# Optimization experiments

Measured on AMD Instinct MI355X. Metric: run time of the kernel, lower is better.

## Reference

```python
import jax, jax.numpy as jnp
import numpy as np

D = 2048
N_PASSES = 2
TOKENS = 16384


def _wht_matrix(d):
    # Sylvester construction of the (unnormalized) Walsh-Hadamard matrix.
    h = np.array([[1.0]], dtype=np.float32)
    while h.shape[0] < d:
        h = np.block([[h, h], [h, -h]])
    return jnp.asarray(h)


def setup_inputs() -> dict:
    key = jax.random.key(0)
    kx, ks = jax.random.split(key)
    x = jax.random.normal(kx, (TOKENS, D), dtype=jnp.float32)
    # random +/-1 sign arrays, one per pass (buffers in the torch module)
    signs = (2 * jax.random.randint(ks, (N_PASSES, D), 0, 2) - 1).astype(jnp.int32)
    wht_mat = _wht_matrix(D)
    return {"x": x, "signs": signs, "wht_mat": wht_mat}


def reference(x, signs, wht_mat):
    # Cascaded SRHT: (sign flip -> dense WHT matmul) x n_passes, scale fused at end.
    final_scale = jnp.asarray(1.0 / (D ** (N_PASSES / 2.0)), dtype=x.dtype)
    s = signs.astype(x.dtype)
    out = x
    for i in range(N_PASSES):
        out = out * s[i]          # [tokens, d] broadcast sign flip
        out = out @ wht_mat       # [tokens, d] x [d, d]
    return out * final_scale
```

## Files before the change

### kernel.cpp

```cpp
#include <hip/hip_runtime.h>

#define DIM 2048

__device__ __forceinline__ int sw(int e) {
  return e ^ (((e >> 7) & 7) << 2);
}

__device__ __forceinline__ float4 sign_flip(float4 v, uint4 s) {
  float4 r;
  r.x = __uint_as_float(__float_as_uint(v.x) ^ (s.x & 0x80000000u));
  r.y = __uint_as_float(__float_as_uint(v.y) ^ (s.y & 0x80000000u));
  r.z = __uint_as_float(__float_as_uint(v.z) ^ (s.z & 0x80000000u));
  r.w = __uint_as_float(__float_as_uint(v.w) ^ (s.w & 0x80000000u));
  return r;
}

#define BFLY(a, b) { float _t = (a); (a) = _t + (b); (b) = _t - (b); }

__device__ __forceinline__ void bf4_pair(float4 &a, float4 &b) {
  BFLY(a.x, b.x); BFLY(a.y, b.y); BFLY(a.z, b.z); BFLY(a.w, b.w);
}

__device__ __forceinline__ void bf_comps(float4 &a) {
  BFLY(a.x, a.y); BFLY(a.z, a.w);
  BFLY(a.x, a.z); BFLY(a.y, a.w);
}

__device__ __forceinline__ void bf_oct(float4 v[8]) {
  bf4_pair(v[0], v[1]); bf4_pair(v[2], v[3]);
  bf4_pair(v[4], v[5]); bf4_pair(v[6], v[7]);
  bf4_pair(v[0], v[2]); bf4_pair(v[1], v[3]);
  bf4_pair(v[4], v[6]); bf4_pair(v[5], v[7]);
  bf4_pair(v[0], v[4]); bf4_pair(v[1], v[5]);
  bf4_pair(v[2], v[6]); bf4_pair(v[3], v[7]);
}

template <int CTRL>
__device__ __forceinline__ float dpp_mov(float x) {
  return __int_as_float(
      __builtin_amdgcn_mov_dpp(__float_as_int(x), CTRL, 0xF, 0xF, true));
}

template <int CTRL>
__device__ __forceinline__ void dpp_stage(float4 v[8], float sgn) {
  #pragma unroll
  for (int i = 0; i < 8; ++i) {
    float px = dpp_mov<CTRL>(v[i].x);
    float py = dpp_mov<CTRL>(v[i].y);
    float pz = dpp_mov<CTRL>(v[i].z);
    float pw = dpp_mov<CTRL>(v[i].w);
    v[i].x = fmaf(sgn, v[i].x, px);
    v[i].y = fmaf(sgn, v[i].y, py);
    v[i].z = fmaf(sgn, v[i].z, pz);
    v[i].w = fmaf(sgn, v[i].w, pw);
  }
}

__global__ __launch_bounds__(256) void srht2_kernel(
    const float* __restrict__ x, const int* __restrict__ signs,
    float* __restrict__ out, int nrows) {
  __shared__ __align__(16) float lds[4][DIM];
  const int lane = threadIdx.x & 63;
  const int wv   = threadIdx.x >> 6;
  const int row  = blockIdx.x * 4 + wv;

  const float sgn1 = (lane & 1) ? -1.0f : 1.0f;
  const float sgn2 = (lane & 2) ? -1.0f : 1.0f;

  const float4* __restrict__ xr = (const float4*)(x + (size_t)row * DIM);
  const uint4*  __restrict__ s0 = (const uint4*)signs;

  float4 v[8];
  #pragma unroll
  for (int c = 0; c < 8; ++c) v[c] = xr[c * 64 + lane];
  #pragma unroll
  for (int c = 0; c < 8; ++c) v[c] = sign_flip(v[c], s0[c * 64 + lane]);

  #pragma unroll
  for (int c = 0; c < 8; ++c) bf_comps(v[c]);
  bf_oct(v);
  dpp_stage<0xB1>(v, sgn1);
  dpp_stage<0x4E>(v, sgn2);

  float* L = lds[wv];
  #pragma unroll
  for (int c = 0; c < 8; ++c)
    *(float4*)(L + sw(c * 256 + lane * 4)) = v[c];
  __syncthreads();

  const int rbase = (((lane >> 1) & 1) << 2) | (((lane >> 2) & 1) << 3)
                  | ((lane & 1) << 7) | ((lane >> 3) << 8);
  float4 w[8];
  #pragma unroll
  for (int j = 0; j < 8; ++j)
    w[j] = *(const float4*)(L + sw(rbase + (j << 4)));

  bf_oct(w);
  dpp_stage<0xB1>(w, sgn1);

  const uint4* __restrict__ s1 = (const uint4*)(signs + DIM);
  #pragma unroll
  for (int j = 0; j < 8; ++j)
    w[j] = sign_flip(w[j], s1[(rbase >> 2) + (j << 2)]);

  #pragma unroll
  for (int j = 0; j < 8; ++j) bf_comps(w[j]);
  bf_oct(w);
  dpp_stage<0xB1>(w, sgn1);
  dpp_stage<0x4E>(w, sgn2);

  __syncthreads();
  #pragma unroll
  for (int j = 0; j < 8; ++j)
    *(float4*)(L + sw(rbase + (j << 4))) = w[j];
  __syncthreads();

  const int rb2 = ((lane & 1) << 3) | (((lane >> 1) & 1) << 2)
                | (((lane >> 2) & 1) << 4) | (((lane >> 3) & 1) << 5)
                | (((lane >> 4) & 1) << 6) | (((lane >> 5) & 1) << 7);
  #pragma unroll
  for (int c = 0; c < 8; ++c)
    v[c] = *(const float4*)(L + sw(rb2 + (c << 8)));

  bf_oct(v);
  dpp_stage<0xB1>(v, sgn1);

  const float sc = 1.0f / 2048.0f;
  float4* __restrict__ orow = (float4*)(out + (size_t)row * DIM);
  #pragma unroll
  for (int c = 0; c < 8; ++c) {
    float4 t = v[c];
    t.x *= sc; t.y *= sc; t.z *= sc; t.w *= sc;
    orow[(rb2 >> 2) + (c << 6)] = t;
  }
}

extern "C" void kernel_launch(void* const* d_in, const int* in_sizes, int n_in,
                              void* d_out, int out_size, void* d_ws, size_t ws_size,
                              hipStream_t stream) {
  const float* x     = (const float*)d_in[0];
  const int*   signs = (const int*)d_in[1];
  float*       out   = (float*)d_out;
  const int nrows   = in_sizes[0] / DIM;
  const int nblocks = nrows / 4;
  hipLaunchKernelGGL(srht2_kernel, dim3(nblocks), dim3(256), 0, stream,
                     x, signs, out, nrows);
}
```

Before: 239.7 us.

## Make waves persistent with register prefetch of next row and packed sign masks

Each wave now runs as a persistent worker that processes several rows with a grid-stride loop, prefetching the next row into registers while it computes the current one. Sign vectors are loaded once per wave and packed into 32-bit bitmasks, so per-row sign loads go away. Block-wide __syncthreads is replaced by wave barriers, since each wave owns its own LDS slice, and output uses nontemporal stores. This costs more registers, which may lower occupancy, and rows_per_wave assumes nrows divides evenly by 4096 waves.

Result: slower. 245.4 us (+2.4%).

```diff
diff --git a/kernel.cpp b/kernel.cpp
--- a/kernel.cpp
+++ b/kernel.cpp
@@ -1,18 +1,20 @@
 #include <hip/hip_runtime.h>
 
 #define DIM 2048
+
+typedef float fvec4 __attribute__((ext_vector_type(4)));
 
 __device__ __forceinline__ int sw(int e) {
   return e ^ (((e >> 7) & 7) << 2);
 }
 
-__device__ __forceinline__ float4 sign_flip(float4 v, uint4 s) {
-  float4 r;
-  r.x = __uint_as_float(__float_as_uint(v.x) ^ (s.x & 0x80000000u));
-  r.y = __uint_as_float(__float_as_uint(v.y) ^ (s.y & 0x80000000u));
-  r.z = __uint_as_float(__float_as_uint(v.z) ^ (s.z & 0x80000000u));
-  r.w = __uint_as_float(__float_as_uint(v.w) ^ (s.w & 0x80000000u));
-  return r;
+__device__ __forceinline__ void wv_fence() {
+  asm volatile("" ::: "memory");
+  __builtin_amdgcn_wave_barrier();
+}
+
+__device__ __forceinline__ float flipbit(float x, unsigned m, int b) {
+  return __uint_as_float(__float_as_uint(x) ^ ((m << (31 - b)) & 0x80000000u));
 }
 
 #define BFLY(a, b) { float _t = (a); (a) = _t + (b); (b) = _t - (b); }
@@ -58,80 +60,124 @@
 
 __global__ __launch_bounds__(256) void srht2_kernel(
     const float* __restrict__ x, const int* __restrict__ signs,
-    float* __restrict__ out, int nrows) {
+    float* __restrict__ out, int rows_per_wave, int total_waves) {
   __shared__ __align__(16) float lds[4][DIM];
   const int lane = threadIdx.x & 63;
   const int wv   = threadIdx.x >> 6;
-  const int row  = blockIdx.x * 4 + wv;
+  const int gw   = blockIdx.x * 4 + wv;
 
   const float sgn1 = (lane & 1) ? -1.0f : 1.0f;
   const float sgn2 = (lane & 2) ? -1.0f : 1.0f;
-
-  const float4* __restrict__ xr = (const float4*)(x + (size_t)row * DIM);
-  const uint4*  __restrict__ s0 = (const uint4*)signs;
-
-  float4 v[8];
-  #pragma unroll
-  for (int c = 0; c < 8; ++c) v[c] = xr[c * 64 + lane];
-  #pragma unroll
-  for (int c = 0; c < 8; ++c) v[c] = sign_flip(v[c], s0[c * 64 + lane]);
-
-  #pragma unroll
-  for (int c = 0; c < 8; ++c) bf_comps(v[c]);
-  bf_oct(v);
-  dpp_stage<0xB1>(v, sgn1);
-  dpp_stage<0x4E>(v, sgn2);
-
   float* L = lds[wv];
-  #pragma unroll
-  for (int c = 0; c < 8; ++c)
-    *(float4*)(L + sw(c * 256 + lane * 4)) = v[c];
-  __syncthreads();
 
   const int rbase = (((lane >> 1) & 1) << 2) | (((lane >> 2) & 1) << 3)
                   | ((lane & 1) << 7) | ((lane >> 3) << 8);
-  float4 w[8];
+  const int rb2   = ((lane & 1) << 3) | (((lane >> 1) & 1) << 2)
+                  | (((lane >> 2) & 1) << 4) | (((lane >> 3) & 1) << 5)
+                  | (((lane >> 4) & 1) << 6) | (((lane >> 5) & 1) << 7);
+
+  const uint4* __restrict__ s0 = (const uint4*)signs;
+  const uint4* __restrict__ s1 = (const uint4*)(signs + DIM);
+  unsigned mask0 = 0u, mask1 = 0u;
   #pragma unroll
-  for (int j = 0; j < 8; ++j)
-    w[j] = *(const float4*)(L + sw(rbase + (j << 4)));
-
-  bf_oct(w);
-  dpp_stage<0xB1>(w, sgn1);
-
-  const uint4* __restrict__ s1 = (const uint4*)(signs + DIM);
-  #pragma unroll
-  for (int j = 0; j < 8; ++j)
-    w[j] = sign_flip(w[j], s1[(rbase >> 2) + (j << 2)]);
-
-  #pragma unroll
-  for (int j = 0; j < 8; ++j) bf_comps(w[j]);
-  bf_oct(w);
-  dpp_stage<0xB1>(w, sgn1);
-  dpp_stage<0x4E>(w, sgn2);
-
-  __syncthreads();
-  #pragma unroll
-  for (int j = 0; j < 8; ++j)
-    *(float4*)(L + sw(rbase + (j << 4))) = w[j];
-  __syncthreads();
-
-  const int rb2 = ((lane & 1) << 3) | (((lane >> 1) & 1) << 2)
-                | (((lane >> 2) & 1) << 4) | (((lane >> 3) & 1) << 5)
-                | (((lane >> 4) & 1) << 6) | (((lane >> 5) & 1) << 7);
-  #pragma unroll
-  for (int c = 0; c < 8; ++c)
-    v[c] = *(const float4*)(L + sw(rb2 + (c << 8)));
-
-  bf_oct(v);
-  dpp_stage<0xB1>(v, sgn1);
+  for (int c = 0; c < 8; ++c) {
+    uint4 u = s0[c * 64 + lane];
+    mask0 |= ((u.x >> 31) << (4 * c)) | ((u.y >> 31) << (4 * c + 1))
+           | ((u.z >> 31) << (4 * c + 2)) | ((u.w >> 31) << (4 * c + 3));
+    uint4 t = s1[(rbase >> 2) + (c << 2)];
+    mask1 |= ((t.x >> 31) << (4 * c)) | ((t.y >> 31) << (4 * c + 1))
+           | ((t.z >> 31) << (4 * c + 2)) | ((t.w >> 31) << (4 * c + 3));
+  }
 
   const float sc = 1.0f / 2048.0f;
-  float4* __restrict__ orow = (float4*)(out + (size_t)row * DIM);
-  #pragma unroll
-  for (int c = 0; c < 8; ++c) {
-    float4 t = v[c];
-    t.x *= sc; t.y *= sc; t.z *= sc; t.w *= sc;
-    orow[(rb2 >> 2) + (c << 6)] = t;
+
+  float4 cur[8];
+  {
+    const float4* xr = (const float4*)(x + (size_t)gw * DIM);
+    #pragma unroll
+    for (int c = 0; c < 8; ++c) cur[c] = xr[c * 64 + lane];
+  }
+
+  #pragma unroll 1
+  for (int i = 0; i < rows_per_wave; ++i) {
+    const int row = gw + i * total_waves;
+
+    float4 nxt[8];
+    if (i + 1 < rows_per_wave) {
+      const float4* xr = (const float4*)(x + (size_t)(row + total_waves) * DIM);
+      #pragma unroll
+      for (int c = 0; c < 8; ++c) nxt[c] = xr[c * 64 + lane];
+    }
+
+    #pragma unroll
+    for (int c = 0; c < 8; ++c) {
+      cur[c].x = flipbit(cur[c].x, mask0, 4 * c + 0);
+      cur[c].y = flipbit(cur[c].y, mask0, 4 * c + 1);
+      cur[c].z = flipbit(cur[c].z, mask0, 4 * c + 2);
+      cur[c].w = flipbit(cur[c].w, mask0, 4 * c + 3);
+    }
+
+    #pragma unroll
+    for (int c = 0; c < 8; ++c) bf_comps(cur[c]);
+    bf_oct(cur);
+    dpp_stage<0xB1>(cur, sgn1);
+    dpp_stage<0x4E>(cur, sgn2);
+
+    wv_fence();
+    #pragma unroll
+    for (int c = 0; c < 8; ++c)
+      *(float4*)(L + sw(c * 256 + lane * 4)) = cur[c];
+    wv_fence();
+    float4 w[8];
+    #pragma unroll
+    for (int j = 0; j < 8; ++j)
+      w[j] = *(const float4*)(L + sw(rbase + (j << 4)));
+    wv_fence();
+
+    bf_oct(w);
+    dpp_stage<0xB1>(w, sgn1);
+
+    #pragma unroll
+    for (int j = 0; j < 8; ++j) {
+      w[j].x = flipbit(w[j].x, mask1, 4 * j + 0);
+      w[j].y = flipbit(w[j].y, mask1, 4 * j + 1);
+      w[j].z = flipbit(w[j].z, mask1, 4 * j + 2);
+      w[j].w = flipbit(w[j].w, mask1, 4 * j + 3);
+    }
+
+    #pragma unroll
+    for (int j = 0; j < 8; ++j) bf_comps(w[j]);
+    bf_oct(w);
+    dpp_stage<0xB1>(w, sgn1);
+    dpp_stage<0x4E>(w, sgn2);
+
+    wv_fence();
+    #pragma unroll
+    for (int j = 0; j < 8; ++j)
+      *(float4*)(L + sw(rbase + (j << 4))) = w[j];
+    wv_fence();
+    float4 v[8];
+    #pragma unroll
+    for (int c = 0; c < 8; ++c)
+      v[c] = *(const float4*)(L + sw(rb2 + (c << 8)));
+    wv_fence();
+
+    bf_oct(v);
+    dpp_stage<0xB1>(v, sgn1);
+
+    fvec4* orow = (fvec4*)(out + (size_t)row * DIM);
+    #pragma unroll
+    for (int c = 0; c < 8; ++c) {
+      fvec4 t;
+      t.x = v[c].x * sc; t.y = v[c].y * sc;
+      t.z = v[c].z * sc; t.w = v[c].w * sc;
+      __builtin_nontemporal_store(t, &orow[(rb2 >> 2) + (c << 6)]);
+    }
+
+    if (i + 1 < rows_per_wave) {
+      #pragma unroll
+      for (int c = 0; c < 8; ++c) cur[c] = nxt[c];
+    }
   }
 }
 
@@ -141,8 +187,10 @@
   const float* x     = (const float*)d_in[0];
   const int*   signs = (const int*)d_in[1];
   float*       out   = (float*)d_out;
-  const int nrows   = in_sizes[0] / DIM;
-  const int nblocks = nrows / 4;
+  const int nrows       = in_sizes[0] / DIM;
+  const int nblocks     = 1024;
+  const int total_waves = nblocks * 4;
+  const int rows_per_wave = nrows / total_waves;
   hipLaunchKernelGGL(srht2_kernel, dim3(nblocks), dim3(256), 0, stream,
-                     x, signs, out, nrows);
+                     x, signs, out, rows_per_wave, total_waves);
 }
```

## Split each row across two waves and pack signs into per-lane bitmasks

Applied to the files above, without the earlier changes.

Each 2048-element row is now handled by two wavefronts of 32 values per lane instead of one wave with 64 per lane. The exchange stages go through LDS with new swizzled scalar writes and float4 reads. A small setup kernel packs the sign arrays into 16-bit per-lane masks, replacing per-element uint4 sign loads with two ushort loads. Output uses nontemporal stores and launch bounds request 8 blocks per CU. The aim is lower register pressure and higher occupancy for this memory-bound transform, at the cost of an extra tiny kernel launch and more scalar LDS traffic.

Result: no change. 240.8 us (+0.5%).

```diff
diff --git a/kernel.cpp b/kernel.cpp
--- a/kernel.cpp
+++ b/kernel.cpp
@@ -2,17 +2,11 @@
 
 #define DIM 2048
 
-__device__ __forceinline__ int sw(int e) {
-  return e ^ (((e >> 7) & 7) << 2);
-}
-
-__device__ __forceinline__ float4 sign_flip(float4 v, uint4 s) {
-  float4 r;
-  r.x = __uint_as_float(__float_as_uint(v.x) ^ (s.x & 0x80000000u));
-  r.y = __uint_as_float(__float_as_uint(v.y) ^ (s.y & 0x80000000u));
-  r.z = __uint_as_float(__float_as_uint(v.z) ^ (s.z & 0x80000000u));
-  r.w = __uint_as_float(__float_as_uint(v.w) ^ (s.w & 0x80000000u));
-  return r;
+typedef float fvec4 __attribute__((ext_vector_type(4)));
+typedef unsigned short ushort_t;
+
+__device__ __forceinline__ float flipbit(float x, unsigned m, int b) {
+  return __uint_as_float(__float_as_uint(x) ^ ((m << (31 - b)) & 0x80000000u));
 }
 
 #define BFLY(a, b) { float _t = (a); (a) = _t + (b); (b) = _t - (b); }
@@ -20,19 +14,13 @@
 __device__ __forceinline__ void bf4_pair(float4 &a, float4 &b) {
   BFLY(a.x, b.x); BFLY(a.y, b.y); BFLY(a.z, b.z); BFLY(a.w, b.w);
 }
-
 __device__ __forceinline__ void bf_comps(float4 &a) {
   BFLY(a.x, a.y); BFLY(a.z, a.w);
   BFLY(a.x, a.z); BFLY(a.y, a.w);
 }
-
-__device__ __forceinline__ void bf_oct(float4 v[8]) {
+__device__ __forceinline__ void bf_quad(float4 v[4]) {
   bf4_pair(v[0], v[1]); bf4_pair(v[2], v[3]);
-  bf4_pair(v[4], v[5]); bf4_pair(v[6], v[7]);
   bf4_pair(v[0], v[2]); bf4_pair(v[1], v[3]);
-  bf4_pair(v[4], v[6]); bf4_pair(v[5], v[7]);
-  bf4_pair(v[0], v[4]); bf4_pair(v[1], v[5]);
-  bf4_pair(v[2], v[6]); bf4_pair(v[3], v[7]);
 }
 
 template <int CTRL>
@@ -40,11 +28,10 @@
   return __int_as_float(
       __builtin_amdgcn_mov_dpp(__float_as_int(x), CTRL, 0xF, 0xF, true));
 }
-
 template <int CTRL>
-__device__ __forceinline__ void dpp_stage(float4 v[8], float sgn) {
-  #pragma unroll
-  for (int i = 0; i < 8; ++i) {
+__device__ __forceinline__ void dpp4(float4 v[4], float sgn) {
+  #pragma unroll
+  for (int i = 0; i < 4; ++i) {
     float px = dpp_mov<CTRL>(v[i].x);
     float py = dpp_mov<CTRL>(v[i].y);
     float pz = dpp_mov<CTRL>(v[i].z);
@@ -56,82 +43,150 @@
   }
 }
 
-__global__ __launch_bounds__(256) void srht2_kernel(
-    const float* __restrict__ x, const int* __restrict__ signs,
-    float* __restrict__ out, int nrows) {
-  __shared__ __align__(16) float lds[4][DIM];
-  const int lane = threadIdx.x & 63;
-  const int wv   = threadIdx.x >> 6;
-  const int row  = blockIdx.x * 4 + wv;
-
-  const float sgn1 = (lane & 1) ? -1.0f : 1.0f;
-  const float sgn2 = (lane & 2) ? -1.0f : 1.0f;
-
-  const float4* __restrict__ xr = (const float4*)(x + (size_t)row * DIM);
-  const uint4*  __restrict__ s0 = (const uint4*)signs;
-
-  float4 v[8];
-  #pragma unroll
-  for (int c = 0; c < 8; ++c) v[c] = xr[c * 64 + lane];
-  #pragma unroll
-  for (int c = 0; c < 8; ++c) v[c] = sign_flip(v[c], s0[c * 64 + lane]);
-
-  #pragma unroll
-  for (int c = 0; c < 8; ++c) bf_comps(v[c]);
-  bf_oct(v);
-  dpp_stage<0xB1>(v, sgn1);
-  dpp_stage<0x4E>(v, sgn2);
-
-  float* L = lds[wv];
-  #pragma unroll
-  for (int c = 0; c < 8; ++c)
-    *(float4*)(L + sw(c * 256 + lane * 4)) = v[c];
+__global__ void mask_setup(const int* __restrict__ signs,
+                           ushort_t* __restrict__ ws) {
+  const int t = threadIdx.x;
+  const int half = (t >> 6) & 1;
+  const int lane = t & 63;
+  unsigned m = 0;
+  if (t < 128) {
+    #pragma unroll
+    for (int k = 0; k < 4; ++k)
+      #pragma unroll
+      for (int c = 0; c < 4; ++c) {
+        int e = (half << 10) | (k << 8) | (lane << 2) | c;
+        m |= (unsigned)(signs[e] < 0) << (k * 4 + c);
+      }
+  } else {
+    const int e10 = lane & 1, e3 = (lane >> 1) & 1, e0 = (lane >> 2) & 1;
+    const int e1 = (lane >> 3) & 1, e2 = (lane >> 4) & 1, e8 = (lane >> 5) & 1;
+    const int base = e0 | (e1 << 1) | (e2 << 2) | (e3 << 3)
+                   | (e8 << 8) | (half << 9) | (e10 << 10);
+    #pragma unroll
+    for (int j = 0; j < 4; ++j)
+      #pragma unroll
+      for (int c = 0; c < 4; ++c) {
+        int e = base | ((c & 1) << 4) | ((c >> 1) << 5)
+                     | ((j & 1) << 6) | ((j >> 1) << 7);
+        m |= (unsigned)(signs[DIM + e] < 0) << (j * 4 + c);
+      }
+  }
+  ws[t] = (ushort_t)m;
+}
+
+__global__ __launch_bounds__(256, 8) void srht2_kernel(
+    const float* __restrict__ x, const ushort_t* __restrict__ masks,
+    float* __restrict__ out) {
+  __shared__ __align__(16) float lds[2][DIM];
+  const int tid  = threadIdx.x;
+  const int lane = tid & 63;
+  const int w    = tid >> 6;
+  const int h    = w & 1;
+  const int rw   = w >> 1;
+  const size_t row = (size_t)blockIdx.x * 2 + rw;
+  float* L = lds[rw];
+
+  const float sgnA = (lane & 1) ? -1.f : 1.f;
+  const float sgnB = (lane & 2) ? -1.f : 1.f;
+
+  const unsigned m0 = masks[(h << 6) | lane];
+  const unsigned m1 = masks[128 + ((h << 6) | lane)];
+
+  const int p0 = lane & 1,        p1 = (lane >> 1) & 1, p2 = (lane >> 2) & 1;
+  const int p3 = (lane >> 3) & 1, p4 = (lane >> 4) & 1, p5 = (lane >> 5) & 1;
+
+  const float4* __restrict__ xr = (const float4*)(x + row * DIM);
+  float4 v[4];
+  #pragma unroll
+  for (int k = 0; k < 4; ++k) v[k] = xr[(h << 8) + (k << 6) + lane];
+
+  #pragma unroll
+  for (int k = 0; k < 4; ++k) {
+    v[k].x = flipbit(v[k].x, m0, 4 * k + 0);
+    v[k].y = flipbit(v[k].y, m0, 4 * k + 1);
+    v[k].z = flipbit(v[k].z, m0, 4 * k + 2);
+    v[k].w = flipbit(v[k].w, m0, 4 * k + 3);
+  }
+  #pragma unroll
+  for (int k = 0; k < 4; ++k) bf_comps(v[k]);
+  bf_quad(v);
+  dpp4<0xB1>(v, sgnA);
+  dpp4<0x4E>(v, sgnB);
+
+  {
+    const int Wb = p2 | (p3 << 1) | ((p4 ^ p0) << 2) | ((p5 ^ p1) << 3)
+                 | (p0 << 6) | (p1 << 7) | (h << 10);
+    #pragma unroll
+    for (int k = 0; k < 4; ++k) {
+      float* p = L + Wb + (k << 8);
+      p[0]  = v[k].x;
+      p[16] = v[k].z;
+      p[32] = v[k].y;
+      p[48] = v[k].w;
+    }
+  }
   __syncthreads();
-
-  const int rbase = (((lane >> 1) & 1) << 2) | (((lane >> 2) & 1) << 3)
-                  | ((lane & 1) << 7) | ((lane >> 3) << 8);
-  float4 w[8];
-  #pragma unroll
-  for (int j = 0; j < 8; ++j)
-    w[j] = *(const float4*)(L + sw(rbase + (j << 4)));
-
-  bf_oct(w);
-  dpp_stage<0xB1>(w, sgn1);
-
-  const uint4* __restrict__ s1 = (const uint4*)(signs + DIM);
-  #pragma unroll
-  for (int j = 0; j < 8; ++j)
-    w[j] = sign_flip(w[j], s1[(rbase >> 2) + (j << 2)]);
-
-  #pragma unroll
-  for (int j = 0; j < 8; ++j) bf_comps(w[j]);
-  bf_oct(w);
-  dpp_stage<0xB1>(w, sgn1);
-  dpp_stage<0x4E>(w, sgn2);
-
+  float4 u[4];
+  {
+    const int R = (p3 << 4) | (p2 << 5) | (p4 << 6) | (p1 << 7)
+                | (p5 << 8) | (h << 9) | (p0 << 10);
+    const int key = p4 | (p1 << 1);
+    #pragma unroll
+    for (int j = 0; j < 4; ++j)
+      u[j] = *(const float4*)(L + R + ((j ^ key) << 2));
+  }
+  #pragma unroll
+  for (int j = 0; j < 4; ++j) bf_comps(u[j]);
+  bf_quad(u);
+  dpp4<0xB1>(u, sgnA);
+  #pragma unroll
+  for (int j = 0; j < 4; ++j) {
+    u[j].x = flipbit(u[j].x, m1, 4 * j + 0);
+    u[j].y = flipbit(u[j].y, m1, 4 * j + 1);
+    u[j].z = flipbit(u[j].z, m1, 4 * j + 2);
+    u[j].w = flipbit(u[j].w, m1, 4 * j + 3);
+  }
+  #pragma unroll
+  for (int j = 0; j < 4; ++j) bf_comps(u[j]);
+  bf_quad(u);
+  dpp4<0xB1>(u, sgnA);
+  dpp4<0x4E>(u, sgnB);
   __syncthreads();
-  #pragma unroll
-  for (int j = 0; j < 8; ++j)
-    *(float4*)(L + sw(rbase + (j << 4))) = w[j];
+  {
+    const int base2 = p2 | (p3 << 1) | (p4 << 8) | (p1 << 9) | (p0 << 10);
+    #pragma unroll
+    for (int j = 0; j < 4; ++j) {
+      const int j0 = j & 1, j1 = j >> 1;
+      float* p = L + (base2 | ((p5 ^ j0) << 2) | ((h ^ j1) << 3)
+                            | (j0 << 6) | (j1 << 7));
+      p[0]  = u[j].x;
+      p[16] = u[j].y;
+      p[32] = u[j].z;
+      p[48] = u[j].w;
+    }
+  }
   __syncthreads();
-
-  const int rb2 = ((lane & 1) << 3) | (((lane >> 1) & 1) << 2)
-                | (((lane >> 2) & 1) << 4) | (((lane >> 3) & 1) << 5)
-                | (((lane >> 4) & 1) << 6) | (((lane >> 5) & 1) << 7);
-  #pragma unroll
-  for (int c = 0; c < 8; ++c)
-    v[c] = *(const float4*)(L + sw(rb2 + (c << 8)));
-
-  bf_oct(v);
-  dpp_stage<0xB1>(v, sgn1);
+  {
+    const int R2 = (p2 << 4) | (p3 << 5) | (p4 << 6) | (p5 << 7)
+                 | (p0 << 8) | (p1 << 9) | (h << 10);
+    const int key2 = p4 | (p5 << 1);
+    #pragma unroll
+    for (int k = 0; k < 4; ++k)
+      v[k] = *(const float4*)(L + R2 + ((k ^ key2) << 2));
+  }
+  #pragma unroll
+  for (int k = 0; k < 4; ++k) bf_comps(v[k]);
+  bf_quad(v);
+  dpp4<0xB1>(v, sgnA);
 
   const float sc = 1.0f / 2048.0f;
-  float4* __restrict__ orow = (float4*)(out + (size_t)row * DIM);
-  #pragma unroll
-  for (int c = 0; c < 8; ++c) {
-    float4 t = v[c];
-    t.x *= sc; t.y *= sc; t.z *= sc; t.w *= sc;
-    orow[(rb2 >> 2) + (c << 6)] = t;
+  fvec4* __restrict__ orow = (fvec4*)(out + row * DIM);
+  #pragma unroll
+  for (int k = 0; k < 4; ++k) {
+    fvec4 t;
+    t.x = v[k].x * sc; t.y = v[k].y * sc;
+    t.z = v[k].z * sc; t.w = v[k].w * sc;
+    __builtin_nontemporal_store(t, &orow[lane + (k << 6) + (h << 8)]);
   }
 }
 
@@ -141,8 +196,11 @@
   const float* x     = (const float*)d_in[0];
   const int*   signs = (const int*)d_in[1];
   float*       out   = (float*)d_out;
+  ushort_t*    ws    = (ushort_t*)d_ws;
   const int nrows   = in_sizes[0] / DIM;
-  const int nblocks = nrows / 4;
+  const int nblocks = nrows / 2;
+
+  hipLaunchKernelGGL(mask_setup, dim3(1), dim3(256), 0, stream, signs, ws);
   hipLaunchKernelGGL(srht2_kernel, dim3(nblocks), dim3(256), 0, stream,
-                     x, signs, out, nrows);
-}
+                     x, ws, out);
+}
```
